# Optimization experiments

Measured on AMD Instinct MI355X. Metric: run time of the kernel, lower is better.

The kernel has to match this reference:

```python
import jax, jax.numpy as jnp
import numpy as np
from jax import lax

DIM = 384
HEADS = 8
HEAD_DIM = DIM // HEADS
EPS = 1e-06


def setup_inputs() -> dict:
    key = jax.random.key(0)
    ks = jax.random.split(key, 16)
    B, N, C = 8, 4096, DIM
    s = 0.02
    inp = {
        "x": jax.random.normal(ks[0], (B, N, C), jnp.float32),
        "wq": jax.random.normal(ks[1], (C, C), jnp.float32) * s,
        "bq": jnp.zeros((C,), jnp.float32),
        "wk": jax.random.normal(ks[2], (C, C), jnp.float32) * s,
        "bk": jnp.zeros((C,), jnp.float32),
        "wv": jax.random.normal(ks[3], (C, C), jnp.float32) * s,
        "bv": jnp.zeros((C,), jnp.float32),
        "wg": jax.random.normal(ks[4], (C, C), jnp.float32) * s,
        "bg": jnp.zeros((C,), jnp.float32),
        "wo": jax.random.normal(ks[5], (C, C), jnp.float32) * s,
        "bo": jnp.zeros((C,), jnp.float32),
        "temperature": jnp.ones((HEADS, 1, 1), jnp.float32),
        "dw_w": jax.random.normal(ks[6], (C, 1, 3, 3), jnp.float32) * s,  # depthwise 3x3
        "dw_b": jnp.zeros((C,), jnp.float32),
        "pw_w": jax.random.normal(ks[7], (C, C), jnp.float32) * s,        # pointwise 1x1
        "pw_b": jnp.zeros((C,), jnp.float32),
    }
    return inp


def _phi(x):
    # exp(x - max) over last dim, numerically stable
    return jnp.exp(x - jnp.max(x, axis=-1, keepdims=True))


def _token_mixer(x, dw_w, dw_b, pw_w, pw_b):
    B, N, C = x.shape
    H = W = int(np.sqrt(N))
    feat = x.transpose(0, 2, 1).reshape(B, C, H, W)
    feat = lax.conv_general_dilated(
        feat, dw_w, window_strides=(1, 1), padding=((1, 1), (1, 1)),
        feature_group_count=C, dimension_numbers=("NCHW", "OIHW", "NCHW"))
    feat = feat + dw_b[None, :, None, None]
    feat = jnp.einsum("bchw,oc->bohw", feat, pw_w) + pw_b[None, :, None, None]
    return feat.reshape(B, C, N).transpose(0, 2, 1)


def reference(x, wq, bq, wk, bk, wv, bv, wg, bg, wo, bo, temperature,
              dw_w, dw_b, pw_w, pw_b):
    B, N, C = x.shape
    residual = x
    x = x + _token_mixer(x, dw_w, dw_b, pw_w, pw_b)

    def heads(y):  # [B,N,C] -> [B,H,N,d]
        return y.reshape(B, N, HEADS, HEAD_DIM).transpose(0, 2, 1, 3)

    q = heads(jnp.einsum("bnc,oc->bno", x, wq) + bq)
    k = heads(jnp.einsum("bnc,oc->bno", x, wk) + bk)
    v = heads(jnp.einsum("bnc,oc->bno", x, wv) + bv)
    g = heads(jnp.einsum("bnc,oc->bno", x, wg) + bg)

    q = _phi(q * temperature[None])       # temperature: [H,1,1] broadcasts over [B,H,N,d]
    k = _phi(k)
    v = v * jax.nn.sigmoid(g)

    kv = jnp.einsum("bhnd,bhne->bhde", k, v)     # [B,H,d,d]
    k_sum = jnp.sum(k, axis=2)                   # [B,H,d]
    num = jnp.einsum("bhnd,bhde->bhne", q, kv)   # [B,H,N,d]
    den = jnp.einsum("bhnd,bhd->bhn", q, k_sum)[..., None] + EPS
    out = num / den

    out = out.transpose(0, 2, 1, 3).reshape(B, N, C)
    out = jnp.einsum("bnc,oc->bno", out, wo) + bo
    return out + 0.0 * residual
```

## Files before the change

kernel.cpp:

```cpp
#include <hip/hip_runtime.h>
#include <math.h>

#define EPSF 1e-6f

typedef __attribute__((ext_vector_type(8))) short bf16x8;
typedef __attribute__((ext_vector_type(4))) float f32x4;
typedef unsigned short u16;
typedef unsigned int u32;

#define MFMA16(a,b,c) __builtin_amdgcn_mfma_f32_16x16x32_bf16((a),(b),(c),0,0,0)

__device__ __forceinline__ u16 f2bf(float f){
  u32 x = __builtin_bit_cast(u32, f);
  u32 r = (x + 0x7fffu + ((x >> 16) & 1u)) >> 16;
  return (u16)r;
}
__device__ __forceinline__ void gll16(const void* g, void* l){
  __builtin_amdgcn_global_load_lds(
      (const __attribute__((address_space(1))) u32*)g,
      (__attribute__((address_space(3))) u32*)l, 16, 0, 0);
}

__global__ __launch_bounds__(256) void k0_prep(
    const float* __restrict__ wq, const float* __restrict__ bq,
    const float* __restrict__ wk, const float* __restrict__ bk,
    const float* __restrict__ wv, const float* __restrict__ bv,
    const float* __restrict__ wg, const float* __restrict__ bg,
    const float* __restrict__ pw_w, const float* __restrict__ wo,
    u16* __restrict__ wpack, u16* __restrict__ pwb, u16* __restrict__ wob,
    float* __restrict__ bpack, float* __restrict__ kvacc, float* __restrict__ ksumacc)
{
  int idx = blockIdx.x*256 + threadIdx.x;
  const int NW = 1536*384;
  if (idx < NW) {
    int r = idx / 384, c = idx - r*384;
    int h = r / 192, s = (r % 192)/48, d = r % 48;
    const float* w = (s==0)?wq:(s==1)?wk:(s==2)?wv:wg;
    wpack[idx] = f2bf(w[(h*48+d)*384 + c]);
    if (c==0){
      const float* b = (s==0)?bq:(s==1)?bk:(s==2)?bv:bg;
      bpack[r] = b[h*48+d];
    }
  } else if (idx < NW + 147456) {
    pwb[idx - NW] = f2bf(pw_w[idx - NW]);
  } else if (idx < NW + 2*147456) {
    wob[idx - NW - 147456] = f2bf(wo[idx - NW - 147456]);
  } else if (idx < NW + 2*147456 + 147456) {
    kvacc[idx - NW - 2*147456] = 0.f;
  } else if (idx < NW + 2*147456 + 147456 + 3072) {
    ksumacc[idx - NW - 2*147456 - 147456] = 0.f;
  }
}

__global__ __launch_bounds__(256) void k1_dw(
    const float* __restrict__ x, const float* __restrict__ dw_w,
    const float* __restrict__ dw_b, u16* __restrict__ t)
{
  int idx = blockIdx.x*256 + threadIdx.x;
  int c4 = idx % 96; int rest = idx / 96;
  int jg = rest & 15; rest >>= 4;
  int i = rest & 63; int b = rest >> 6;
  int c0 = c4*4, j0 = jg*4;
  float wf[36];
  {
    const float4* wp = (const float4*)(dw_w + c0*9);
    #pragma unroll
    for (int k=0;k<9;k++){
      float4 v = wp[k];
      wf[4*k] = v.x; wf[4*k+1] = v.y; wf[4*k+2] = v.z; wf[4*k+3] = v.w;
    }
  }
  float4 bias = *(const float4*)(dw_b + c0);
  float acc[4][4];
  #pragma unroll
  for (int tk=0;tk<4;tk++){
    acc[tk][0]=bias.x; acc[tk][1]=bias.y; acc[tk][2]=bias.z; acc[tk][3]=bias.w;
  }
  const float* xb = x + ((size_t)b<<12)*384;
  #pragma unroll
  for (int di=-1; di<=1; ++di){
    int ii = i+di; if ((unsigned)ii >= 64u) continue;
    #pragma unroll
    for (int dj=-1; dj<=4; ++dj){
      int jj = j0+dj; if ((unsigned)jj >= 64u) continue;
      float4 xv = *(const float4*)(xb + (size_t)((ii<<6)+jj)*384 + c0);
      #pragma unroll
      for (int tk=0;tk<4;tk++){
        const int dd = dj - tk;
        if (dd < -1 || dd > 1) continue;
        const int tap = (di+1)*3 + (dd+1);
        acc[tk][0] = fmaf(xv.x, wf[0*9+tap], acc[tk][0]);
        acc[tk][1] = fmaf(xv.y, wf[1*9+tap], acc[tk][1]);
        acc[tk][2] = fmaf(xv.z, wf[2*9+tap], acc[tk][2]);
        acc[tk][3] = fmaf(xv.w, wf[3*9+tap], acc[tk][3]);
      }
    }
  }
  int mbase = (b<<12) + (i<<6) + j0;
  #pragma unroll
  for (int tk=0;tk<4;tk++){
    ushort4 o; o.x=f2bf(acc[tk][0]); o.y=f2bf(acc[tk][1]);
    o.z=f2bf(acc[tk][2]); o.w=f2bf(acc[tk][3]);
    *(ushort4*)(t + (size_t)(mbase+tk)*384 + c0) = o;
  }
}

__global__ __launch_bounds__(256) void k2_gemm_pw(
    const u16* __restrict__ t, const u16* __restrict__ pwb,
    const float* __restrict__ x, const float* __restrict__ pw_b,
    u16* __restrict__ xm)
{
  __shared__ __align__(16) u16 As[128*64];
  __shared__ __align__(16) u16 Bs[128*64];
  const int m0 = blockIdx.x * 128;
  const int n0 = blockIdx.y * 128;
  const int tid = threadIdx.x, w = tid>>6, l = tid&63;
  const int lc = l & 15, hi = l >> 4;
  const int osw = ((l&7) ^ (l>>3))*16;
  const f32x4 zf = {0.f,0.f,0.f,0.f};
  f32x4 acc[4][4];
  #pragma unroll
  for (int i=0;i<4;i++)
    #pragma unroll
    for (int j=0;j<4;j++) acc[i][j] = zf;

  for (int k0=0; k0<384; k0+=64) {
    #pragma unroll
    for (int i=0;i<4;i++){
      int ch = w*4+i;
      int row = ch*8 + (l>>3);
      gll16((const char*)t   + ((size_t)(m0+row)*384 + k0)*2 + osw, (char*)As + ch*1024);
      gll16((const char*)pwb + ((size_t)(n0+row)*384 + k0)*2 + osw, (char*)Bs + ch*1024);
    }
    __syncthreads();
    const int wr = (w>>1)*64, wc = (w&1)*64;
    #pragma unroll
    for (int kk=0; kk<64; kk+=32){
      const int sc = (((kk>>3)+hi) ^ (lc&7))*8;
      bf16x8 a[4], bb[4];
      #pragma unroll
      for (int i=0;i<4;i++) a[i]  = *(const bf16x8*)&As[(wr + i*16 + lc)*64 + sc];
      #pragma unroll
      for (int j=0;j<4;j++) bb[j] = *(const bf16x8*)&Bs[(wc + j*16 + lc)*64 + sc];
      #pragma unroll
      for (int i=0;i<4;i++)
        #pragma unroll
        for (int j=0;j<4;j++)
          acc[i][j] = MFMA16(a[i], bb[j], acc[i][j]);
    }
    __syncthreads();
  }
  const int wr=(w>>1)*64, wc=(w&1)*64;
  #pragma unroll
  for (int j=0;j<4;j++){
    int n = n0 + wc + j*16 + lc;
    float bias = pw_b[n];
    #pragma unroll
    for (int i=0;i<4;i++)
      #pragma unroll
      for (int r=0;r<4;r++){
        int m = m0 + wr + i*16 + hi*4 + r;
        float v = acc[i][j][r] + x[(size_t)m*384 + n] + bias;
        xm[(size_t)m*384 + n] = f2bf(v);
      }
  }
}

__global__ __launch_bounds__(256) void k3_gemm_qkvg(
    const u16* __restrict__ xm, const u16* __restrict__ wpack,
    const float* __restrict__ bpack, const float* __restrict__ temperature,
    u16* __restrict__ qh, float* __restrict__ kvacc, float* __restrict__ ksumacc)
{
  __shared__ __align__(16) u16 smem[20480];
  u16* As = smem;
  u16* Bs = smem + 8192;
  const int m0 = blockIdx.x * 128;
  const int h  = blockIdx.y;
  const int tid = threadIdx.x, w = tid>>6, l = tid&63;
  const int lc = l & 15, hi = l >> 4;
  const int osw = ((l&7) ^ (l>>3))*16;
  const f32x4 zf = {0.f,0.f,0.f,0.f};
  f32x4 acc[2][12];
  #pragma unroll
  for (int i=0;i<2;i++)
    #pragma unroll
    for (int j=0;j<12;j++) acc[i][j] = zf;

  for (int k0=0; k0<384; k0+=64){
    #pragma unroll
    for (int i=0;i<4;i++){
      int ch = w*4+i, row = ch*8 + (l>>3);
      gll16((const char*)xm + ((size_t)(m0+row)*384 + k0)*2 + osw, (char*)As + ch*1024);
    }
    #pragma unroll
    for (int i=0;i<6;i++){
      int ch = w*6+i, row = ch*8 + (l>>3);
      gll16((const char*)wpack + ((size_t)(h*192+row)*384 + k0)*2 + osw, (char*)Bs + ch*1024);
    }
    __syncthreads();
    const int rbase = w*32;
    #pragma unroll
    for (int kk=0; kk<64; kk+=32){
      const int sc = (((kk>>3)+hi) ^ (lc&7))*8;
      bf16x8 a0 = *(const bf16x8*)&As[(rbase +      lc)*64 + sc];
      bf16x8 a1 = *(const bf16x8*)&As[(rbase + 16 + lc)*64 + sc];
      #pragma unroll
      for (int j=0;j<12;j++){
        bf16x8 bb = *(const bf16x8*)&Bs[(j*16 + lc)*64 + sc];
        acc[0][j] = MFMA16(a0, bb, acc[0][j]);
        acc[1][j] = MFMA16(a1, bb, acc[1][j]);
      }
    }
    __syncthreads();
  }

  const float tq = temperature[h];
  const int b = m0 >> 12;
  const size_t bh = (size_t)b*8 + h;
  const int bb0 = h*192;
  float biasq[3], biask[3], biasv[3], biasg[3];
  #pragma unroll
  for (int j=0;j<3;j++){
    biasq[j] = bpack[bb0       + j*16 + lc];
    biask[j] = bpack[bb0 + 48  + j*16 + lc];
    biasv[j] = bpack[bb0 + 96  + j*16 + lc];
    biasg[j] = bpack[bb0 + 144 + j*16 + lc];
  }
  u16* kT = smem;
  u16* vT = smem + 6528;
  float ksp[3] = {0.f, 0.f, 0.f};

  #pragma unroll
  for (int i=0;i<2;i++){
    ushort4 kst[3], vst[3];
    #pragma unroll
    for (int r=0;r<4;r++){
      int m = m0 + w*32 + i*16 + hi*4 + r;
      int n = m & 4095;
      size_t rowq = (bh*4096 + n)*64;
      float q0=(acc[i][0][r]+biasq[0])*tq;
      float q1=(acc[i][1][r]+biasq[1])*tq;
      float q2=(acc[i][2][r]+biasq[2])*tq;
      float mx = fmaxf(q0,fmaxf(q1,q2));
      mx = fmaxf(mx, __shfl_xor(mx,1,64));
      mx = fmaxf(mx, __shfl_xor(mx,2,64));
      mx = fmaxf(mx, __shfl_xor(mx,4,64));
      mx = fmaxf(mx, __shfl_xor(mx,8,64));
      qh[rowq +      lc] = f2bf(expf(q0-mx));
      qh[rowq + 16 + lc] = f2bf(expf(q1-mx));
      qh[rowq + 32 + lc] = f2bf(expf(q2-mx));
      qh[rowq + 48 + lc] = 0;
      float s0=acc[i][3][r]+biask[0];
      float s1=acc[i][4][r]+biask[1];
      float s2=acc[i][5][r]+biask[2];
      float mk = fmaxf(s0,fmaxf(s1,s2));
      mk = fmaxf(mk, __shfl_xor(mk,1,64));
      mk = fmaxf(mk, __shfl_xor(mk,2,64));
      mk = fmaxf(mk, __shfl_xor(mk,4,64));
      mk = fmaxf(mk, __shfl_xor(mk,8,64));
      float k0e = expf(s0-mk), k1e = expf(s1-mk), k2e = expf(s2-mk);
      ksp[0] += k0e; ksp[1] += k1e; ksp[2] += k2e;
      u16 kq0=f2bf(k0e), kq1=f2bf(k1e), kq2=f2bf(k2e);
      u16 vq[3];
      #pragma unroll
      for (int j=0;j<3;j++){
        float vv = acc[i][6+j][r] + biasv[j];
        float gg = acc[i][9+j][r] + biasg[j];
        float sg = 1.f/(1.f + expf(-gg));
        vq[j] = f2bf(vv*sg);
      }
      if (r==0){ kst[0].x=kq0; kst[1].x=kq1; kst[2].x=kq2; vst[0].x=vq[0]; vst[1].x=vq[1]; vst[2].x=vq[2]; }
      if (r==1){ kst[0].y=kq0; kst[1].y=kq1; kst[2].y=kq2; vst[0].y=vq[0]; vst[1].y=vq[1]; vst[2].y=vq[2]; }
      if (r==2){ kst[0].z=kq0; kst[1].z=kq1; kst[2].z=kq2; vst[0].z=vq[0]; vst[1].z=vq[1]; vst[2].z=vq[2]; }
      if (r==3){ kst[0].w=kq0; kst[1].w=kq1; kst[2].w=kq2; vst[0].w=vq[0]; vst[1].w=vq[1]; vst[2].w=vq[2]; }
    }
    int mb = w*32 + i*16 + hi*4;
    #pragma unroll
    for (int j=0;j<3;j++){
      *(ushort4*)&kT[(j*16+lc)*136 + mb] = kst[j];
      *(ushort4*)&vT[(j*16+lc)*136 + mb] = vst[j];
    }
  }
  __syncthreads();

  bf16x8 af[3], bfv[3];
  #pragma unroll
  for (int da=0;da<3;da++) af[da]  = *(const bf16x8*)&kT[(da*16+lc)*136 + w*32 + hi*8];
  #pragma unroll
  for (int eb=0;eb<3;eb++) bfv[eb] = *(const bf16x8*)&vT[(eb*16+lc)*136 + w*32 + hi*8];
  f32x4 a2[3][3];
  #pragma unroll
  for (int da=0;da<3;da++)
    #pragma unroll
    for (int eb=0;eb<3;eb++)
      a2[da][eb] = MFMA16(af[da], bfv[eb], zf);
  __syncthreads();
  float* pb = (float*)smem + w*2304;
  #pragma unroll
  for (int da=0;da<3;da++)
    #pragma unroll
    for (int eb=0;eb<3;eb++)
      #pragma unroll
      for (int rr=0;rr<4;rr++)
        pb[(da*16 + hi*4 + rr)*48 + eb*16 + lc] = a2[da][eb][rr];
  __syncthreads();
  float* p0 = (float*)smem;
  for (int u=tid; u<2304; u+=256){
    float s = p0[u] + p0[2304+u] + p0[4608+u] + p0[6912+u];
    atomicAdd(kvacc + bh*2304 + u, s);
  }
  #pragma unroll
  for (int j=0;j<3;j++){
    ksp[j] += __shfl_xor(ksp[j],16,64);
    ksp[j] += __shfl_xor(ksp[j],32,64);
  }
  if (hi==0){
    atomicAdd(ksumacc + bh*48 +      lc, ksp[0]);
    atomicAdd(ksumacc + bh*48 + 16 + lc, ksp[1]);
    atomicAdd(ksumacc + bh*48 + 32 + lc, ksp[2]);
  }
}

__global__ __launch_bounds__(256) void k5_red(
    const float* __restrict__ kvacc, const float* __restrict__ ksumacc,
    u16* __restrict__ kvp)
{
  int bh = blockIdx.x, tid = threadIdx.x;
  for (int u=tid; u<4096; u+=256){
    int e = u >> 6, d = u & 63;
    float v = 0.f;
    if (e < 48 && d < 48)       v = kvacc[(size_t)bh*2304 + d*48 + e];
    else if (e == 48 && d < 48) v = ksumacc[bh*48 + d];
    kvp[((size_t)bh*64 + e)*64 + d] = f2bf(v);
  }
}

__global__ __launch_bounds__(256) void k6_num(
    const u16* __restrict__ qh, const u16* __restrict__ kvp, u16* __restrict__ ah)
{
  __shared__ __align__(16) u16 As[256*64];
  __shared__ __align__(16) u16 Bs[64*64];
  const int bh = blockIdx.x >> 4, nc = blockIdx.x & 15;
  const int tid = threadIdx.x, w = tid>>6, l = tid&63;
  const int lc = l & 15, hi = l >> 4;
  const f32x4 zf = {0.f,0.f,0.f,0.f};
  const u16* gq = qh + ((size_t)bh*4096 + nc*256)*64;
  #pragma unroll
  for (int it=0; it<8; ++it){
    int s = it*256 + tid;
    int row = s>>3, c = s&7, g = c ^ (row&7);
    ((uint4*)As)[s] = *(const uint4*)(gq + (size_t)row*64 + g*8);
  }
  const u16* gk = kvp + (size_t)bh*4096;
  #pragma unroll
  for (int it=0; it<2; ++it){
    int s = it*256 + tid;
    int row = s>>3, c = s&7, g = c ^ (row&7);
    ((uint4*)Bs)[s] = *(const uint4*)(gk + (size_t)row*64 + g*8);
  }
  __syncthreads();
  f32x4 acc[4][4];
  #pragma unroll
  for (int i=0;i<4;i++)
    #pragma unroll
    for (int j=0;j<4;j++) acc[i][j] = zf;
  const int rbase = w*64;
  #pragma unroll
  for (int kk=0; kk<64; kk+=32){
    const int sc = (((kk>>3)+hi) ^ (lc&7))*8;
    bf16x8 a[4], bb[4];
    #pragma unroll
    for (int i=0;i<4;i++) a[i]  = *(const bf16x8*)&As[(rbase + i*16 + lc)*64 + sc];
    #pragma unroll
    for (int j=0;j<4;j++) bb[j] = *(const bf16x8*)&Bs[(j*16 + lc)*64 + sc];
    #pragma unroll
    for (int i=0;i<4;i++)
      #pragma unroll
      for (int j=0;j<4;j++)
        acc[i][j] = MFMA16(a[i], bb[j], acc[i][j]);
  }
  const int b = bh >> 3, h = bh & 7;
  #pragma unroll
  for (int i=0;i<4;i++){
    #pragma unroll
    for (int r=0;r<4;r++){
      float den = __shfl(acc[i][3][r], l & 48, 64) + EPSF;
      float rd = 1.f/den;
      int n = nc*256 + rbase + i*16 + hi*4 + r;
      size_t ob = ((size_t)b*4096 + n)*384 + h*48;
      ah[ob +      lc] = f2bf(acc[i][0][r]*rd);
      ah[ob + 16 + lc] = f2bf(acc[i][1][r]*rd);
      ah[ob + 32 + lc] = f2bf(acc[i][2][r]*rd);
    }
  }
}

__global__ __launch_bounds__(256) void k7_gemm_out(
    const u16* __restrict__ ah, const u16* __restrict__ wob,
    const float* __restrict__ bo, float* __restrict__ out)
{
  __shared__ __align__(16) u16 As[128*64];
  __shared__ __align__(16) u16 Bs[128*64];
  const int m0 = blockIdx.x * 128;
  const int n0 = blockIdx.y * 128;
  const int tid = threadIdx.x, w = tid>>6, l = tid&63;
  const int lc = l & 15, hi = l >> 4;
  const int osw = ((l&7) ^ (l>>3))*16;
  const f32x4 zf = {0.f,0.f,0.f,0.f};
  f32x4 acc[4][4];
  #pragma unroll
  for (int i=0;i<4;i++)
    #pragma unroll
    for (int j=0;j<4;j++) acc[i][j] = zf;

  for (int k0=0; k0<384; k0+=64) {
    #pragma unroll
    for (int i=0;i<4;i++){
      int ch = w*4+i;
      int row = ch*8 + (l>>3);
      gll16((const char*)ah  + ((size_t)(m0+row)*384 + k0)*2 + osw, (char*)As + ch*1024);
      gll16((const char*)wob + ((size_t)(n0+row)*384 + k0)*2 + osw, (char*)Bs + ch*1024);
    }
    __syncthreads();
    const int wr = (w>>1)*64, wc = (w&1)*64;
    #pragma unroll
    for (int kk=0; kk<64; kk+=32){
      const int sc = (((kk>>3)+hi) ^ (lc&7))*8;
      bf16x8 a[4], bb[4];
      #pragma unroll
      for (int i=0;i<4;i++) a[i]  = *(const bf16x8*)&As[(wr + i*16 + lc)*64 + sc];
      #pragma unroll
      for (int j=0;j<4;j++) bb[j] = *(const bf16x8*)&Bs[(wc + j*16 + lc)*64 + sc];
      #pragma unroll
      for (int i=0;i<4;i++)
        #pragma unroll
        for (int j=0;j<4;j++)
          acc[i][j] = MFMA16(a[i], bb[j], acc[i][j]);
    }
    __syncthreads();
  }
  const int wr=(w>>1)*64, wc=(w&1)*64;
  #pragma unroll
  for (int j=0;j<4;j++){
    int n = n0 + wc + j*16 + lc;
    float bias = bo[n];
    #pragma unroll
    for (int i=0;i<4;i++)
      #pragma unroll
      for (int r=0;r<4;r++){
        int m = m0 + wr + i*16 + hi*4 + r;
        out[(size_t)m*384 + n] = acc[i][j][r] + bias;
      }
  }
}

extern "C" void kernel_launch(void* const* d_in, const int* in_sizes, int n_in,
                              void* d_out, int out_size, void* d_ws, size_t ws_size,
                              hipStream_t stream)
{
  const float* x    = (const float*)d_in[0];
  const float* wq   = (const float*)d_in[1];
  const float* bq   = (const float*)d_in[2];
  const float* wk   = (const float*)d_in[3];
  const float* bk   = (const float*)d_in[4];
  const float* wv   = (const float*)d_in[5];
  const float* bv   = (const float*)d_in[6];
  const float* wg   = (const float*)d_in[7];
  const float* bg   = (const float*)d_in[8];
  const float* wo   = (const float*)d_in[9];
  const float* bo   = (const float*)d_in[10];
  const float* temp = (const float*)d_in[11];
  const float* dw_w = (const float*)d_in[12];
  const float* dw_b = (const float*)d_in[13];
  const float* pw_w = (const float*)d_in[14];
  const float* pw_b = (const float*)d_in[15];
  float* out = (float*)d_out;
  char* ws = (char*)d_ws;

  u16*   t       = (u16*)(ws + 0);
  u16*   xm      = (u16*)(ws + 25165824);
  u16*   qh      = (u16*)(ws + 50331648);
  u16*   wpack   = (u16*)(ws + 83886080);
  u16*   pwb     = (u16*)(ws + 85065728);
  u16*   wob     = (u16*)(ws + 85360640);
  float* bpack   = (float*)(ws + 85655552);
  float* kvacc   = (float*)(ws + 85661696);
  float* ksumacc = (float*)(ws + 86251520);
  u16*   kvp     = (u16*)(ws + 86263808);

  k0_prep<<<4044, 256, 0, stream>>>(wq,bq,wk,bk,wv,bv,wg,bg,pw_w,wo,
                                    wpack,pwb,wob,bpack,kvacc,ksumacc);
  k1_dw<<<3072, 256, 0, stream>>>(x, dw_w, dw_b, t);
  k2_gemm_pw<<<dim3(256,3), 256, 0, stream>>>(t, pwb, x, pw_b, xm);
  k3_gemm_qkvg<<<dim3(256,8), 256, 0, stream>>>(xm, wpack, bpack, temp, qh, kvacc, ksumacc);
  k5_red<<<64, 256, 0, stream>>>(kvacc, ksumacc, kvp);
  k6_num<<<1024, 256, 0, stream>>>(qh, kvp, t );
  k7_gemm_out<<<dim3(256,3), 256, 0, stream>>>(t, wob, bo, out);
}
```

Measured before the change: 193.3 us.

## Double-buffer shared-memory tiles in QKVG GEMM to overlap loads with MFMA

```diff
diff --git a/kernel.cpp b/kernel.cpp
--- a/kernel.cpp
+++ b/kernel.cpp
@@ -171,9 +171,7 @@
     const float* __restrict__ bpack, const float* __restrict__ temperature,
     u16* __restrict__ qh, float* __restrict__ kvacc, float* __restrict__ ksumacc)
 {
-  __shared__ __align__(16) u16 smem[20480];
-  u16* As = smem;
-  u16* Bs = smem + 8192;
+  __shared__ __align__(16) u16 smem[40960];
   const int m0 = blockIdx.x * 128;
   const int h  = blockIdx.y;
   const int tid = threadIdx.x, w = tid>>6, l = tid&63;
@@ -186,33 +184,47 @@
     #pragma unroll
     for (int j=0;j<12;j++) acc[i][j] = zf;
 
-  for (int k0=0; k0<384; k0+=64){
-    #pragma unroll
-    for (int i=0;i<4;i++){
-      int ch = w*4+i, row = ch*8 + (l>>3);
-      gll16((const char*)xm + ((size_t)(m0+row)*384 + k0)*2 + osw, (char*)As + ch*1024);
-    }
-    #pragma unroll
-    for (int i=0;i<6;i++){
-      int ch = w*6+i, row = ch*8 + (l>>3);
-      gll16((const char*)wpack + ((size_t)(h*192+row)*384 + k0)*2 + osw, (char*)Bs + ch*1024);
-    }
-    __syncthreads();
-    const int rbase = w*32;
+  const int arow = (w*4)*8 + (l>>3);
+  const int brow = (w*6)*8 + (l>>3);
+
+  #define K3_STAGE(T, BUF) do {                                                \
+    const int k0_ = (T)*64;                                                    \
+    char* Ab_ = (char*)(smem + (BUF)*8192);                                    \
+    char* Bb_ = (char*)(smem + 16384 + (BUF)*12288);                           \
+    _Pragma("unroll")                                                          \
+    for (int i=0;i<4;i++)                                                      \
+      gll16((const char*)xm + ((size_t)(m0+arow+i*8)*384 + k0_)*2 + osw,       \
+            Ab_ + (w*4+i)*1024);                                               \
+    _Pragma("unroll")                                                          \
+    for (int i=0;i<6;i++)                                                      \
+      gll16((const char*)wpack + ((size_t)(h*192+brow+i*8)*384 + k0_)*2 + osw, \
+            Bb_ + (w*6+i)*1024);                                               \
+  } while(0)
+
+  K3_STAGE(0, 0);
+  __syncthreads();
+  int cur = 0;
+  const int rbase = w*32;
+  for (int t=0; t<6; ++t){
+    if (t < 5) K3_STAGE(t+1, cur^1);
+    const u16* Ab = smem + cur*8192;
+    const u16* Bb = smem + 16384 + cur*12288;
     #pragma unroll
     for (int kk=0; kk<64; kk+=32){
       const int sc = (((kk>>3)+hi) ^ (lc&7))*8;
-      bf16x8 a0 = *(const bf16x8*)&As[(rbase +      lc)*64 + sc];
-      bf16x8 a1 = *(const bf16x8*)&As[(rbase + 16 + lc)*64 + sc];
+      bf16x8 a0 = *(const bf16x8*)&Ab[(rbase +      lc)*64 + sc];
+      bf16x8 a1 = *(const bf16x8*)&Ab[(rbase + 16 + lc)*64 + sc];
       #pragma unroll
       for (int j=0;j<12;j++){
-        bf16x8 bb = *(const bf16x8*)&Bs[(j*16 + lc)*64 + sc];
+        bf16x8 bb = *(const bf16x8*)&Bb[(j*16 + lc)*64 + sc];
         acc[0][j] = MFMA16(a0, bb, acc[0][j]);
         acc[1][j] = MFMA16(a1, bb, acc[1][j]);
       }
     }
     __syncthreads();
-  }
+    cur ^= 1;
+  }
+  #undef K3_STAGE
 
   const float tq = temperature[h];
   const int b = m0 >> 12;
```

New measurement: 190.9 us. About the same (-1.2%).
